# Performance work log

Hardware: AMD Instinct MI355X
Metric: run time of the kernel (lower is better)

## Reference

```python
import jax, jax.numpy as jnp
import numpy as np

KS = 3   # kernel_size
PAD = 1  # padding
N_K = KS * KS


def conv2d(x, w, b=None, stride=1, pad=0):
    out = jax.lax.conv_general_dilated(
        x, w, (stride, stride), [(pad, pad), (pad, pad)],
        dimension_numbers=('NCHW', 'OIHW', 'NCHW'))
    if b is not None:
        out = out + b[None, :, None, None]
    return out


def deform_sample(x, offset):
    # x: [b,c,H,W]  offset: [b,2N,h,w] -> [b,c,h,w,N]
    b, c, H, W = x.shape
    _, twoN, h, w = offset.shape
    N = twoN // 2
    xp = jnp.pad(x, ((0, 0), (0, 0), (PAD, PAD), (PAD, PAD)))
    Hp, Wp = H + 2 * PAD, W + 2 * PAD
    r = (KS - 1) // 2
    knx, kny = jnp.meshgrid(jnp.arange(-r, r + 1), jnp.arange(-r, r + 1), indexing='ij')
    pnx = knx.reshape(-1).astype(offset.dtype)  # [N] kernel x offsets
    pny = kny.reshape(-1).astype(offset.dtype)
    off = jnp.transpose(offset, (0, 2, 3, 1))   # [b,h,w,2N]
    p0x = (jnp.arange(h) + PAD).astype(offset.dtype)
    p0y = (jnp.arange(w) + PAD).astype(offset.dtype)
    px = p0x[None, :, None, None] + pnx[None, None, None, :] + off[..., :N]  # [b,h,w,N]
    py = p0y[None, None, :, None] + pny[None, None, None, :] + off[..., N:]
    # q = p.detach().floor() in torch -> stop_gradient here
    flx = jnp.floor(jax.lax.stop_gradient(px))
    fly = jnp.floor(jax.lax.stop_gradient(py))
    qltx = jnp.clip(flx, 0, Hp - 1)
    qrbx = jnp.clip(flx + 1, 0, Hp - 1)
    qlty = jnp.clip(fly, 0, Wp - 1)
    qrby = jnp.clip(fly + 1, 0, Wp - 1)
    pxc = jnp.clip(px, 0, Hp - 1)
    pyc = jnp.clip(py, 0, Wp - 1)
    g_lt = (1 + (qltx - pxc)) * (1 + (qlty - pyc))
    g_rb = (1 - (qrbx - pxc)) * (1 - (qrby - pyc))
    g_lb = (1 - (qrbx - pxc)) * (1 + (qlty - pyc))
    g_rt = (1 + (qltx - pxc)) * (1 - (qrby - pyc))
    ix_lt, ix_rb = qltx.astype(jnp.int32), qrbx.astype(jnp.int32)
    iy_lt, iy_rb = qlty.astype(jnp.int32), qrby.astype(jnp.int32)

    def gather(ix, iy):
        def one(xb, ixb, iyb):
            return xb[:, ixb, iyb]  # [c,h,w,N]
        return jax.vmap(one)(xp, ix, iy)

    x_lt = gather(ix_lt, iy_lt)
    x_rb = gather(ix_rb, iy_rb)
    x_lb = gather(ix_rb, iy_lt)
    x_rt = gather(ix_lt, iy_rb)
    return (g_lt[:, None] * x_lt + g_rb[:, None] * x_rb
            + g_lb[:, None] * x_lb + g_rt[:, None] * x_rt)


def z_weight(z, mode):
    # cubic interpolation basis weights; z: [b,N,h,w] -> [b,1,h,w,N]
    if mode == '1':
        w = 1 - 11.0 / 6.0 * z + z ** 2 - 1.0 / 6.0 * z ** 3
    elif mode == '2':
        w = 3 * z - 2.5 * z ** 2 + 0.5 * z ** 3
    elif mode == '4':
        w = -1.5 * z + 2 * z ** 2 - 0.5 * z ** 3
    else:
        w = 1.0 / 3.0 * z - 0.5 * z ** 2 + 1.0 / 6.0 * z ** 3
    return jnp.transpose(w, (0, 2, 3, 1))[:, None]


def reshape_x_offset(xo):
    # [b,c,h,w,ks*ks] -> [b,c,h*ks,w*ks] (torch cat/view equivalent)
    b, c, h, w, _ = xo.shape
    xo = xo.reshape(b, c, h, w, KS, KS)          # N = g*ks + k
    xo = jnp.transpose(xo, (0, 1, 2, 4, 3, 5))   # (b,c,h,g,w,k)
    return xo.reshape(b, c, h * KS, w * KS)


def setup_inputs() -> dict:
    key = jax.random.key(0)
    ks = jax.random.split(key, 18)
    B, C, OSC, OUTC, H, W = 2, 64, 64, 64, 128, 128
    f = jax.random.normal
    inp = {
        'img1': f(ks[0], (B, C, H, W), jnp.float32),
        'img2': f(ks[1], (B, C, H, W), jnp.float32),
        'img4': f(ks[2], (B, C, H, W), jnp.float32),
        'img5': f(ks[3], (B, C, H, W), jnp.float32),
        'offset_source': f(ks[4], (B, OSC, H, W), jnp.float32),
        'w_pc1': f(ks[5], (2 * N_K, OSC, 5, 5), jnp.float32) * 0.01,
        'b_pc1': f(ks[6], (2 * N_K,), jnp.float32) * 0.01,
        'w_pc2': f(ks[7], (2 * N_K, OSC, 5, 5), jnp.float32) * 0.01,
        'b_pc2': f(ks[8], (2 * N_K,), jnp.float32) * 0.01,
        'w_pc4': f(ks[9], (2 * N_K, OSC, 5, 5), jnp.float32) * 0.01,
        'b_pc4': f(ks[10], (2 * N_K,), jnp.float32) * 0.01,
        'w_pc5': f(ks[11], (2 * N_K, OSC, 5, 5), jnp.float32) * 0.01,
        'b_pc5': f(ks[12], (2 * N_K,), jnp.float32) * 0.01,
        'w_z': f(ks[13], (N_K, OSC, 5, 5), jnp.float32) * 0.01,
        'b_z': f(ks[14], (N_K,), jnp.float32) * 0.01,
        'w_m': f(ks[15], (N_K, OSC, 5, 5), jnp.float32) * 0.01,
        'b_m': f(ks[16], (N_K,), jnp.float32) * 0.01,
        'w_conv': f(ks[17], (OUTC, C, KS, KS), jnp.float32) * 0.05,
    }
    return inp


def reference(img1, img2, img4, img5, offset_source,
              w_pc1, b_pc1, w_pc2, b_pc2, w_pc4, b_pc4, w_pc5, b_pc5,
              w_z, b_z, w_m, b_m, w_conv):
    off1 = conv2d(offset_source, w_pc1, b_pc1, pad=2)
    off2 = conv2d(offset_source, w_pc2, b_pc2, pad=2)
    off4 = conv2d(offset_source, w_pc4, b_pc4, pad=2)
    off5 = conv2d(offset_source, w_pc5, b_pc5, pad=2)
    z = 3.0 * jax.nn.sigmoid(conv2d(offset_source, w_z, b_z, pad=2))
    m = jax.nn.sigmoid(conv2d(offset_source, w_m, b_m, pad=2))
    f1 = deform_sample(img1, off1)
    f2 = deform_sample(img2, off2)
    f4 = deform_sample(img4, off4)
    f5 = deform_sample(img5, off5)
    central = (f1 * z_weight(z, '1') + f2 * z_weight(z, '2')
               + f4 * z_weight(z, '4') + f5 * z_weight(z, '5'))
    central = central * jnp.transpose(m, (0, 2, 3, 1))[:, None]
    out = conv2d(reshape_x_offset(central), w_conv, None, stride=KS)
    return out
```

## Files before the change

kernel.cpp:

```cpp
#include <hip/hip_runtime.h>
#include <hip/hip_bf16.h>
#include <math.h>

#define HWX 16384

typedef __attribute__((ext_vector_type(8))) short short8v;
typedef __attribute__((ext_vector_type(4))) float f32x4;

__device__ inline ushort f2bf(float x) {
    union { __hip_bfloat16 h; ushort u; } cv;
    cv.h = __float2bfloat16(x);
    return cv.u;
}

__global__ __launch_bounds__(256) void packw_kernel(
    const float* __restrict__ w1, const float* __restrict__ b1,
    const float* __restrict__ w2, const float* __restrict__ b2,
    const float* __restrict__ w4, const float* __restrict__ b4,
    const float* __restrict__ w5, const float* __restrict__ b5,
    const float* __restrict__ wz, const float* __restrict__ bz,
    const float* __restrict__ wm, const float* __restrict__ bm,
    __hip_bfloat16* __restrict__ Wpk, float* __restrict__ bpack)
{
    const int idx = blockIdx.x * 256 + threadIdx.x;
    if (idx < 96) {
        const int o = idx; float v = 0.f;
        if      (o < 18) v = b1[o];
        else if (o < 36) v = b2[o - 18];
        else if (o < 54) v = b4[o - 36];
        else if (o < 72) v = b5[o - 54];
        else if (o < 81) v = bz[o - 72];
        else if (o < 90) v = bm[o - 81];
        bpack[o] = v;
    }
    if (idx < 96 * 1600) {
        const int o   = idx / 1600;
        const int k   = idx - o * 1600;
        const int kyx = k >> 6;
        const int ic  = k & 63;
        const int off = ic * 25 + kyx;
        float v = 0.f;
        if      (o < 18) v = w1[o * 1600 + off];
        else if (o < 36) v = w2[(o - 18) * 1600 + off];
        else if (o < 54) v = w4[(o - 36) * 1600 + off];
        else if (o < 72) v = w5[(o - 54) * 1600 + off];
        else if (o < 81) v = wz[(o - 72) * 1600 + off];
        else if (o < 90) v = wm[(o - 81) * 1600 + off];
        Wpk[idx] = __float2bfloat16(v);
    }
}

__global__ __launch_bounds__(256) void packosT_kernel(
    const float* __restrict__ src, __hip_bfloat16* __restrict__ osT)
{
    const int yy = blockIdx.x;
    const int b  = blockIdx.y;
    __hip_bfloat16* dst = osT + ((size_t)b * 132 + yy) * 132 * 64;
    for (int idx = threadIdx.x; idx < 132 * 64; idx += 256) {
        const int xx = idx >> 6;
        const int c  = idx & 63;
        float v = 0.f;
        if (yy >= 2 && yy < 130 && xx >= 2 && xx < 130)
            v = src[(((b << 6) + c) << 14) + ((yy - 2) << 7) + (xx - 2)];
        dst[idx] = __float2bfloat16(v);
    }
}

__global__ __launch_bounds__(256) void conv_mfma_kernel(
    const __hip_bfloat16* __restrict__ Wpk,
    const float* __restrict__ bpack,
    const __hip_bfloat16* __restrict__ osT,
    float* __restrict__ offs,
    float* __restrict__ zbuf,
    float* __restrict__ mbuf)
{
    __shared__ __align__(16) ushort slab[5 * 68 * 64];
    __shared__ __align__(16) ushort wbuf[2][96 * 64];

    const int bx = blockIdx.x;
    const int y  = bx >> 1;
    const int x0 = (bx & 1) << 6;
    const int b  = blockIdx.y;
    const int t    = threadIdx.x;
    const int wv   = t >> 6;
    const int lane = t & 63;
    const int l15  = lane & 15;
    const int kgrp = lane >> 4;
    const int wm   = wv >> 1;
    const int wn   = wv & 1;

    const ushort* ob = (const ushort*)osT + (size_t)b * (132 * 132 * 64);
    const ushort* Wg = (const ushort*)Wpk;

    for (int c = t; c < 2720; c += 256) {
        const int r5  = c / 544;
        const int rem = c - r5 * 544;
        const int col = rem >> 3;
        const int cb  = rem & 7;
        const short8v v = *(const short8v*)(ob + (((y + r5) * 132 + x0 + col) << 6) + (cb << 3));
        const int slot = r5 * 544 + (col << 3) + (cb ^ (col & 7));
        *(short8v*)((char*)slab + slot * 16) = v;
    }

#define STAGE_W(kyx, bi)                                                       \
    _Pragma("unroll")                                                          \
    for (int it = 0; it < 3; ++it) {                                           \
        const int c  = it * 256 + t;                                           \
        const int oc = c >> 3, cb = c & 7;                                     \
        const ushort* src = Wg + oc * 1600 + (kyx) * 64 + ((cb ^ (oc & 7)) << 3); \
        __builtin_amdgcn_global_load_lds(                                      \
            (const __attribute__((address_space(1))) void*)src,                \
            (__attribute__((address_space(3))) void*)((char*)wbuf[bi] + (it * 256 + wv * 64) * 16), \
            16, 0, 0);                                                         \
    }

    STAGE_W(0, 0)
    __syncthreads();

    f32x4 acc[3][2];
    #pragma unroll
    for (int m = 0; m < 3; ++m)
        #pragma unroll
        for (int n = 0; n < 2; ++n) acc[m][n] = (f32x4){0.f, 0.f, 0.f, 0.f};

    for (int kyx = 0; kyx < 25; ++kyx) {
        const int bi = kyx & 1;
        if (kyx < 24) STAGE_W(kyx + 1, bi ^ 1)
        const int ky = kyx / 5, kx = kyx % 5;
        #pragma unroll
        for (int kc = 0; kc < 2; ++kc) {
            const int kcg = (kc << 2) + kgrp;
            short8v af[3], bf[2];
            #pragma unroll
            for (int m = 0; m < 3; ++m) {
                const int oc = wm * 48 + m * 16 + l15;
                af[m] = *(const short8v*)((char*)wbuf[bi] + ((oc << 3) + (kcg ^ (oc & 7))) * 16);
            }
            #pragma unroll
            for (int n = 0; n < 2; ++n) {
                const int col = wn * 32 + n * 16 + l15 + kx;
                bf[n] = *(const short8v*)((char*)slab + ((ky * 68 + col) * 8 + (kcg ^ (col & 7))) * 16);
            }
            #pragma unroll
            for (int m = 0; m < 3; ++m)
                #pragma unroll
                for (int n = 0; n < 2; ++n)
                    acc[m][n] = __builtin_amdgcn_mfma_f32_16x16x32_bf16(af[m], bf[n], acc[m][n], 0, 0, 0);
        }
        __syncthreads();
    }
#undef STAGE_W

    #pragma unroll
    for (int m = 0; m < 3; ++m) {
        const int ocb = wm * 48 + m * 16 + (kgrp << 2);
        #pragma unroll
        for (int n = 0; n < 2; ++n) {
            const int x = x0 + wn * 32 + n * 16 + l15;
            const int p = (y << 7) + x;
            #pragma unroll
            for (int r = 0; r < 4; ++r) {
                const int o = ocb + r;
                const float v = acc[m][n][r] + bpack[o];
                if (o < 72) {
                    const int i = o / 18, ch = o - i * 18;
                    offs[i * (2 * 18 * HWX) + (((b * 18) + ch) << 14) + p] = v;
                } else if (o < 81) {
                    zbuf[((b * 9 + (o - 72)) << 14) + p] = 3.f / (1.f + expf(-v));
                } else if (o < 90) {
                    mbuf[((b * 9 + (o - 81)) << 14) + p] = 1.f / (1.f + expf(-v));
                }
            }
        }
    }
}

__global__ __launch_bounds__(256) void transpose_kernel(
    const float* __restrict__ i0, const float* __restrict__ i1,
    const float* __restrict__ i2, const float* __restrict__ i3,
    ushort* __restrict__ imgT)
{
    const int img = blockIdx.z;
    const int b   = blockIdx.y;
    const int p0  = blockIdx.x << 6;
    const float* src = (img == 0) ? i0 : (img == 1) ? i1 : (img == 2) ? i2 : i3;

    __shared__ float tile[64][65];
    const int t = threadIdx.x;
    const int pp = t & 63, c0 = t >> 6;
    #pragma unroll
    for (int k = 0; k < 16; ++k) {
        const int c = (k << 2) + c0;
        tile[c][pp] = src[(((b << 6) + c) << 14) + p0 + pp];
    }
    __syncthreads();
    const int c2 = t & 31, pl = t >> 5;
    #pragma unroll
    for (int k = 0; k < 8; ++k) {
        const int pi = (k << 3) + pl;
        const uint packed = (uint)f2bf(tile[2 * c2][pi])
                          | ((uint)f2bf(tile[2 * c2 + 1][pi]) << 16);
        *(uint*)(imgT + ((size_t)(((img << 1) + b) << 14) + p0 + pi) * 64 + 2 * c2)
            = packed;
    }
}

__global__ __launch_bounds__(256) void wcpk_kernel(
    const float* __restrict__ wc, __hip_bfloat16* __restrict__ WcPk)
{
    const int idx = blockIdx.x * 256 + threadIdx.x;
    if (idx < 36864) WcPk[idx] = __float2bfloat16(wc[idx]);
}

__global__ __launch_bounds__(256, 5) void fused_kernel(
    const float* __restrict__ offs,
    const float* __restrict__ zbuf,
    const float* __restrict__ mbuf,
    const ushort* __restrict__ imgT,
    const __hip_bfloat16* __restrict__ WcPk,
    float* __restrict__ out)
{
    __shared__ __hip_bfloat16 s_sb[16 * 584];
    __shared__ ushort4 s_ti[16 * 36];
    __shared__ float4  s_tw4[16 * 36];

    const int t   = threadIdx.x;
    const int pid = blockIdx.x;
    const int b   = pid >> 10;
    const int rem = pid & 1023;
    const int h   = rem >> 3;
    const int w0p = (rem & 7) << 4;

    for (int u = t; u < 576; u += 256) {
        const int px   = u / 36;
        const int unit = u - px * 36;
        const int i    = unit / 9;
        const int n    = unit - i * 9;
        const int wcol = w0p + px;
        const int p    = (h << 7) + wcol;

        const float* ob = offs + i * (2 * 18 * HWX) + ((b * 18) << 14);
        const float ox = ob[(n << 14) + p];
        const float oy = ob[((n + 9) << 14) + p];
        const float z  = zbuf[((b * 9 + n) << 14) + p];
        const float mm = mbuf[((b * 9 + n) << 14) + p];

        const float zc0 = (i == 0) ? 1.f : 0.f;
        const float zc1 = (i == 0) ? (-11.f / 6.f) : (i == 1) ? 3.f
                         : (i == 2) ? -1.5f : (1.f / 3.f);
        const float zc2 = (i == 0) ? 1.f : (i == 1) ? -2.5f
                         : (i == 2) ? 2.f : -0.5f;
        const float zc3 = (i == 0) ? (-1.f / 6.f) : (i == 1) ? 0.5f
                         : (i == 2) ? -0.5f : (1.f / 6.f);
        const float zw   = zc0 + z * (zc1 + z * (zc2 + z * zc3));
        const float coef = zw * mm;

        const float pxf = (float)(h + n / 3) + ox;
        const float pyf = (float)(wcol + n % 3) + oy;
        const float flx = floorf(pxf), fly = floorf(pyf);
        const float qltx = fminf(fmaxf(flx, 0.f), 129.f);
        const float qrbx = fminf(fmaxf(flx + 1.f, 0.f), 129.f);
        const float qlty = fminf(fmaxf(fly, 0.f), 129.f);
        const float qrby = fminf(fmaxf(fly + 1.f, 0.f), 129.f);
        const float pxc = fminf(fmaxf(pxf, 0.f), 129.f);
        const float pyc = fminf(fmaxf(pyf, 0.f), 129.f);
        const float gxl = 1.f + (qltx - pxc);
        const float gxr = 1.f - (qrbx - pxc);
        const float gyl = 1.f + (qlty - pyc);
        const float gyr = 1.f - (qrby - pyc);
        const int ixl = (int)qltx, ixr = (int)qrbx;
        const int iyl = (int)qlty, iyr = (int)qrby;

        ushort4 ti; float4 tw;
        auto mk = [&](int qx, int qy, float g, ushort& ii, float& ww) {
            const bool valid = (qx >= 1) && (qx <= 128) && (qy >= 1) && (qy <= 128);
            ii = (ushort)(valid ? (((qx - 1) << 7) + (qy - 1)) : 0);
            ww = valid ? g * coef : 0.f;
        };
        mk(ixl, iyl, gxl * gyl, ti.x, tw.x);
        mk(ixr, iyr, gxr * gyr, ti.y, tw.y);
        mk(ixr, iyl, gxr * gyl, ti.z, tw.z);
        mk(ixl, iyr, gxl * gyr, ti.w, tw.w);
        s_ti[u]  = ti;
        s_tw4[u] = tw;
    }
    __syncthreads();

    const int lane = t & 63;
    const int wv   = t >> 6;
    const int c4   = lane & 15;
    const int pxs  = lane >> 4;
    const int px   = (wv << 2) + pxs;

    f32x4 s4[9];
    #pragma unroll
    for (int n = 0; n < 9; ++n) s4[n] = (f32x4){0.f, 0.f, 0.f, 0.f};

    const int tb = px * 36;
    #pragma unroll 1
    for (int i = 0; i < 4; ++i) {
        const char* ibl = (const char*)(imgT + (((size_t)((i << 1) + b)) << 20)) + (c4 << 3);
        #pragma unroll
        for (int n = 0; n < 9; ++n) {
            const ushort4 tib = s_ti[tb + i * 9 + n];
            const float4  tw  = s_tw4[tb + i * 9 + n];
            {
                const uint2 v = *(const uint2*)(ibl + ((uint)tib.x << 7));
                s4[n].x = fmaf(tw.x, __uint_as_float(v.x << 16),         s4[n].x);
                s4[n].y = fmaf(tw.x, __uint_as_float(v.x & 0xffff0000u), s4[n].y);
                s4[n].z = fmaf(tw.x, __uint_as_float(v.y << 16),         s4[n].z);
                s4[n].w = fmaf(tw.x, __uint_as_float(v.y & 0xffff0000u), s4[n].w);
            }
            {
                const uint2 v = *(const uint2*)(ibl + ((uint)tib.y << 7));
                s4[n].x = fmaf(tw.y, __uint_as_float(v.x << 16),         s4[n].x);
                s4[n].y = fmaf(tw.y, __uint_as_float(v.x & 0xffff0000u), s4[n].y);
                s4[n].z = fmaf(tw.y, __uint_as_float(v.y << 16),         s4[n].z);
                s4[n].w = fmaf(tw.y, __uint_as_float(v.y & 0xffff0000u), s4[n].w);
            }
            {
                const uint2 v = *(const uint2*)(ibl + ((uint)tib.z << 7));
                s4[n].x = fmaf(tw.z, __uint_as_float(v.x << 16),         s4[n].x);
                s4[n].y = fmaf(tw.z, __uint_as_float(v.x & 0xffff0000u), s4[n].y);
                s4[n].z = fmaf(tw.z, __uint_as_float(v.y << 16),         s4[n].z);
                s4[n].w = fmaf(tw.z, __uint_as_float(v.y & 0xffff0000u), s4[n].w);
            }
            {
                const uint2 v = *(const uint2*)(ibl + ((uint)tib.w << 7));
                s4[n].x = fmaf(tw.w, __uint_as_float(v.x << 16),         s4[n].x);
                s4[n].y = fmaf(tw.w, __uint_as_float(v.x & 0xffff0000u), s4[n].y);
                s4[n].z = fmaf(tw.w, __uint_as_float(v.y << 16),         s4[n].z);
                s4[n].w = fmaf(tw.w, __uint_as_float(v.y & 0xffff0000u), s4[n].w);
            }
        }
    }

    uint bufu[18];
    #pragma unroll
    for (int k = 0; k < 18; ++k) {
        const int u0 = 2 * k, u1 = 2 * k + 1;
        const float v0 = s4[u0 % 9][u0 / 9];
        const float v1 = s4[u1 % 9][u1 / 9];
        bufu[k] = (uint)f2bf(v0) | ((uint)f2bf(v1) << 16);
    }
    {
        uint2* dst = (uint2*)((char*)s_sb + px * 1168 + c4 * 72);
        #pragma unroll
        for (int k = 0; k < 9; ++k)
            dst[k] = ((const uint2*)bufu)[k];
    }
    __syncthreads();

    const int l15  = lane & 15;
    const int kgrp = lane >> 4;
    const ushort* Wb = (const ushort*)WcPk + (wv * 16 + l15) * 576 + kgrp * 8;
    const ushort* sb = (const ushort*)s_sb + l15 * 584 + kgrp * 8;

    f32x4 acc = {0.f, 0.f, 0.f, 0.f};
    #pragma unroll
    for (int ks = 0; ks < 18; ++ks) {
        const short8v a  = *(const short8v*)(Wb + ks * 32);
        const short8v bb = *(const short8v*)(sb + ks * 32);
        acc = __builtin_amdgcn_mfma_f32_16x16x32_bf16(a, bb, acc, 0, 0, 0);
    }

    const int p = (h << 7) + w0p + l15;
    #pragma unroll
    for (int r = 0; r < 4; ++r) {
        const int oc = wv * 16 + (kgrp << 2) + r;
        out[(((b << 6) + oc) << 14) + p] = acc[r];
    }
}

extern "C" void kernel_launch(void* const* d_in, const int* in_sizes, int n_in,
                              void* d_out, int out_size, void* d_ws, size_t ws_size,
                              hipStream_t stream) {
    (void)in_sizes; (void)n_in; (void)out_size; (void)ws_size;
    const float* img1  = (const float*)d_in[0];
    const float* img2  = (const float*)d_in[1];
    const float* img4  = (const float*)d_in[2];
    const float* img5  = (const float*)d_in[3];
    const float* osrc  = (const float*)d_in[4];
    const float* w_pc1 = (const float*)d_in[5];
    const float* b_pc1 = (const float*)d_in[6];
    const float* w_pc2 = (const float*)d_in[7];
    const float* b_pc2 = (const float*)d_in[8];
    const float* w_pc4 = (const float*)d_in[9];
    const float* b_pc4 = (const float*)d_in[10];
    const float* w_pc5 = (const float*)d_in[11];
    const float* b_pc5 = (const float*)d_in[12];
    const float* w_z   = (const float*)d_in[13];
    const float* b_z   = (const float*)d_in[14];
    const float* w_m   = (const float*)d_in[15];
    const float* b_m   = (const float*)d_in[16];
    const float* w_cv  = (const float*)d_in[17];
    float* out = (float*)d_out;

    float* wsf  = (float*)d_ws;
    float* offs = wsf;
    float* zbuf = wsf + 4 * 589824;
    float* mbuf = zbuf + 294912;
    float* WcTr = mbuf + 294912;
    float* imgTr = WcTr + 36864;

    __hip_bfloat16* WcPk  = (__hip_bfloat16*)WcTr;
    ushort*         imgTb = (ushort*)imgTr;

    __hip_bfloat16* Wpk   = (__hip_bfloat16*)imgTr;
    float*          bpack = imgTr + 76800;
    __hip_bfloat16* osT   = (__hip_bfloat16*)(imgTr + 76912);

    packw_kernel<<<dim3((96 * 1600 + 255) / 256), 256, 0, stream>>>(
        w_pc1, b_pc1, w_pc2, b_pc2, w_pc4, b_pc4, w_pc5, b_pc5,
        w_z, b_z, w_m, b_m, Wpk, bpack);
    packosT_kernel<<<dim3(132, 2), 256, 0, stream>>>(osrc, osT);
    conv_mfma_kernel<<<dim3(256, 2), 256, 0, stream>>>(
        Wpk, bpack, osT, offs, zbuf, mbuf);
    transpose_kernel<<<dim3(256, 2, 4), 256, 0, stream>>>(img1, img2, img4, img5, imgTb);
    wcpk_kernel<<<dim3(144), 256, 0, stream>>>(w_cv, WcPk);
    fused_kernel<<<dim3(2048), 256, 0, stream>>>(offs, zbuf, mbuf, imgTb, WcPk, out);
}
```

Before: 118.4 us.

## Swizzle block IDs for XCD locality and pack bilinear taps into bf16

Remaps block indices in the transpose and fused kernels so consecutive work items land on the same XCD (blockIdx & 7 chooses the chunk), so each XCD's L2 holds one batch's image slice and its gathered neighbours. Also packs the four tap indices and four bilinear weights into one uint4 per tap, with the weights stored as bf16, which halves the shared-memory footprint and LDS reads in the gather loop. Rounding the weights to bf16 adds extra precision loss on top of the existing bf16 image data.

```diff
diff --git a/kernel.cpp b/kernel.cpp
--- a/kernel.cpp
+++ b/kernel.cpp
@@ -180,9 +180,12 @@
     const float* __restrict__ i2, const float* __restrict__ i3,
     ushort* __restrict__ imgT)
 {
-    const int img = blockIdx.z;
-    const int b   = blockIdx.y;
-    const int p0  = blockIdx.x << 6;
+    const int wid = ((blockIdx.x & 7) << 8) + (blockIdx.x >> 3);
+    const int xcd = wid >> 8;
+    const int j   = wid & 255;
+    const int img = j >> 6;
+    const int b   = xcd >> 2;
+    const int p0  = ((((xcd & 3) << 6) + (j & 63)) << 6);
     const float* src = (img == 0) ? i0 : (img == 1) ? i1 : (img == 2) ? i2 : i3;
 
     __shared__ float tile[64][65];
@@ -221,11 +224,10 @@
     float* __restrict__ out)
 {
     __shared__ __hip_bfloat16 s_sb[16 * 584];
-    __shared__ ushort4 s_ti[16 * 36];
-    __shared__ float4  s_tw4[16 * 36];
+    __shared__ uint4 s_tap[16 * 36];
 
     const int t   = threadIdx.x;
-    const int pid = blockIdx.x;
+    const int pid = ((blockIdx.x & 7) << 8) + (blockIdx.x >> 3);
     const int b   = pid >> 10;
     const int rem = pid & 1023;
     const int h   = rem >> 3;
@@ -271,18 +273,22 @@
         const int ixl = (int)qltx, ixr = (int)qrbx;
         const int iyl = (int)qlty, iyr = (int)qrby;
 
-        ushort4 ti; float4 tw;
-        auto mk = [&](int qx, int qy, float g, ushort& ii, float& ww) {
+        uint i0, i1, i2, i3, u0, u1, u2, u3;
+        auto mk = [&](int qx, int qy, float g, uint& ii, uint& ww) {
             const bool valid = (qx >= 1) && (qx <= 128) && (qy >= 1) && (qy <= 128);
-            ii = (ushort)(valid ? (((qx - 1) << 7) + (qy - 1)) : 0);
-            ww = valid ? g * coef : 0.f;
+            ii = valid ? (uint)(((qx - 1) << 7) + (qy - 1)) : 0u;
+            ww = valid ? (uint)f2bf(g * coef) : 0u;
         };
-        mk(ixl, iyl, gxl * gyl, ti.x, tw.x);
-        mk(ixr, iyr, gxr * gyr, ti.y, tw.y);
-        mk(ixr, iyl, gxr * gyl, ti.z, tw.z);
-        mk(ixl, iyr, gxl * gyr, ti.w, tw.w);
-        s_ti[u]  = ti;
-        s_tw4[u] = tw;
+        mk(ixl, iyl, gxl * gyl, i0, u0);
+        mk(ixr, iyr, gxr * gyr, i1, u1);
+        mk(ixr, iyl, gxr * gyl, i2, u2);
+        mk(ixl, iyr, gxl * gyr, i3, u3);
+        uint4 tp;
+        tp.x = i0 | (i1 << 16);
+        tp.y = i2 | (i3 << 16);
+        tp.z = u0 | (u1 << 16);
+        tp.w = u2 | (u3 << 16);
+        s_tap[u] = tp;
     }
     __syncthreads();
 
@@ -302,35 +308,38 @@
         const char* ibl = (const char*)(imgT + (((size_t)((i << 1) + b)) << 20)) + (c4 << 3);
         #pragma unroll
         for (int n = 0; n < 9; ++n) {
-            const ushort4 tib = s_ti[tb + i * 9 + n];
-            const float4  tw  = s_tw4[tb + i * 9 + n];
+            const uint4 tp = s_tap[tb + i * 9 + n];
+            const float w0 = __uint_as_float(tp.z << 16);
+            const float w1 = __uint_as_float(tp.z & 0xffff0000u);
+            const float w2 = __uint_as_float(tp.w << 16);
+            const float w3 = __uint_as_float(tp.w & 0xffff0000u);
             {
-                const uint2 v = *(const uint2*)(ibl + ((uint)tib.x << 7));
-                s4[n].x = fmaf(tw.x, __uint_as_float(v.x << 16),         s4[n].x);
-                s4[n].y = fmaf(tw.x, __uint_as_float(v.x & 0xffff0000u), s4[n].y);
-                s4[n].z = fmaf(tw.x, __uint_as_float(v.y << 16),         s4[n].z);
-                s4[n].w = fmaf(tw.x, __uint_as_float(v.y & 0xffff0000u), s4[n].w);
+                const uint2 v = *(const uint2*)(ibl + ((tp.x & 0xffffu) << 7));
+                s4[n].x = fmaf(w0, __uint_as_float(v.x << 16),         s4[n].x);
+                s4[n].y = fmaf(w0, __uint_as_float(v.x & 0xffff0000u), s4[n].y);
+                s4[n].z = fmaf(w0, __uint_as_float(v.y << 16),         s4[n].z);
+                s4[n].w = fmaf(w0, __uint_as_float(v.y & 0xffff0000u), s4[n].w);
             }
             {
-                const uint2 v = *(const uint2*)(ibl + ((uint)tib.y << 7));
-                s4[n].x = fmaf(tw.y, __uint_as_float(v.x << 16),         s4[n].x);
-                s4[n].y = fmaf(tw.y, __uint_as_float(v.x & 0xffff0000u), s4[n].y);
-                s4[n].z = fmaf(tw.y, __uint_as_float(v.y << 16),         s4[n].z);
-                s4[n].w = fmaf(tw.y, __uint_as_float(v.y & 0xffff0000u), s4[n].w);
+                const uint2 v = *(const uint2*)(ibl + ((tp.x >> 16) << 7));
+                s4[n].x = fmaf(w1, __uint_as_float(v.x << 16),         s4[n].x);
+                s4[n].y = fmaf(w1, __uint_as_float(v.x & 0xffff0000u), s4[n].y);
+                s4[n].z = fmaf(w1, __uint_as_float(v.y << 16),         s4[n].z);
+                s4[n].w = fmaf(w1, __uint_as_float(v.y & 0xffff0000u), s4[n].w);
             }
             {
-                const uint2 v = *(const uint2*)(ibl + ((uint)tib.z << 7));
-                s4[n].x = fmaf(tw.z, __uint_as_float(v.x << 16),         s4[n].x);
-                s4[n].y = fmaf(tw.z, __uint_as_float(v.x & 0xffff0000u), s4[n].y);
-                s4[n].z = fmaf(tw.z, __uint_as_float(v.y << 16),         s4[n].z);
-                s4[n].w = fmaf(tw.z, __uint_as_float(v.y & 0xffff0000u), s4[n].w);
+                const uint2 v = *(const uint2*)(ibl + ((tp.y & 0xffffu) << 7));
+                s4[n].x = fmaf(w2, __uint_as_float(v.x << 16),         s4[n].x);
+                s4[n].y = fmaf(w2, __uint_as_float(v.x & 0xffff0000u), s4[n].y);
+                s4[n].z = fmaf(w2, __uint_as_float(v.y << 16),         s4[n].z);
+                s4[n].w = fmaf(w2, __uint_as_float(v.y & 0xffff0000u), s4[n].w);
             }
             {
-                const uint2 v = *(const uint2*)(ibl + ((uint)tib.w << 7));
-                s4[n].x = fmaf(tw.w, __uint_as_float(v.x << 16),         s4[n].x);
-                s4[n].y = fmaf(tw.w, __uint_as_float(v.x & 0xffff0000u), s4[n].y);
-                s4[n].z = fmaf(tw.w, __uint_as_float(v.y << 16),         s4[n].z);
-                s4[n].w = fmaf(tw.w, __uint_as_float(v.y & 0xffff0000u), s4[n].w);
+                const uint2 v = *(const uint2*)(ibl + ((tp.y >> 16) << 7));
+                s4[n].x = fmaf(w3, __uint_as_float(v.x << 16),         s4[n].x);
+                s4[n].y = fmaf(w3, __uint_as_float(v.x & 0xffff0000u), s4[n].y);
+                s4[n].z = fmaf(w3, __uint_as_float(v.y << 16),         s4[n].z);
+                s4[n].w = fmaf(w3, __uint_as_float(v.y & 0xffff0000u), s4[n].w);
             }
         }
     }
@@ -416,7 +425,7 @@
     packosT_kernel<<<dim3(132, 2), 256, 0, stream>>>(osrc, osT);
     conv_mfma_kernel<<<dim3(256, 2), 256, 0, stream>>>(
         Wpk, bpack, osT, offs, zbuf, mbuf);
-    transpose_kernel<<<dim3(256, 2, 4), 256, 0, stream>>>(img1, img2, img4, img5, imgTb);
+    transpose_kernel<<<dim3(2048), 256, 0, stream>>>(img1, img2, img4, img5, imgTb);
     wcpk_kernel<<<dim3(144), 256, 0, stream>>>(w_cv, WcPk);
     fused_kernel<<<dim3(2048), 256, 0, stream>>>(offs, zbuf, mbuf, imgTb, WcPk, out);
 }
```

Measured after the change: 124.3 us. 1.05x slower.

## Split fused gather+GEMM into separate gather and MFMA kernels, pack tap weights as bf16

Applied to the files above, without the earlier changes.

When the workspace is large enough, the fused deformable-sample plus output-conv kernel is split in two. A gather kernel writes the sampled bf16 columns to global memory with an XOR swizzle. An sgemm kernel then loads those columns into LDS via global_load_lds and runs the MFMA reduction. Tap indices and weights are now packed into one uint4 per tap, with the weights in bf16, which halves LDS tap storage but lowers the precision of the bilinear weights. The split adds a roughly 38MB global round trip and an extra launch, in exchange for lower register and LDS pressure in each kernel.

```diff
diff --git a/kernel.cpp b/kernel.cpp
--- a/kernel.cpp
+++ b/kernel.cpp
@@ -70,9 +70,7 @@
     const __hip_bfloat16* __restrict__ Wpk,
     const float* __restrict__ bpack,
     const __hip_bfloat16* __restrict__ osT,
-    float* __restrict__ offs,
-    float* __restrict__ zbuf,
-    float* __restrict__ mbuf)
+    float* __restrict__ offs, float* __restrict__ zbuf, float* __restrict__ mbuf)
 {
     __shared__ __align__(16) ushort slab[5 * 68 * 64];
     __shared__ __align__(16) ushort wbuf[2][96 * 64];
@@ -212,17 +210,121 @@
     if (idx < 36864) WcPk[idx] = __float2bfloat16(wc[idx]);
 }
 
-__global__ __launch_bounds__(256, 5) void fused_kernel(
-    const float* __restrict__ offs,
-    const float* __restrict__ zbuf,
-    const float* __restrict__ mbuf,
-    const ushort* __restrict__ imgT,
-    const __hip_bfloat16* __restrict__ WcPk,
-    float* __restrict__ out)
-{
-    __shared__ __hip_bfloat16 s_sb[16 * 584];
-    __shared__ ushort4 s_ti[16 * 36];
-    __shared__ float4  s_tw4[16 * 36];
+#define TAP_PHASE_A(S_TAP)                                                     \
+    for (int u = t; u < 576; u += 256) {                                       \
+        const int px_  = u / 36;                                               \
+        const int unit = u - px_ * 36;                                         \
+        const int i    = unit / 9;                                             \
+        const int n    = unit - i * 9;                                         \
+        const int wcol = w0p + px_;                                            \
+        const int p    = (h << 7) + wcol;                                      \
+        const float* ob = offs + i * (2 * 18 * HWX) + ((b * 18) << 14);        \
+        const float ox = ob[(n << 14) + p];                                    \
+        const float oy = ob[((n + 9) << 14) + p];                              \
+        const float z  = zbuf[((b * 9 + n) << 14) + p];                        \
+        const float mm = mbuf[((b * 9 + n) << 14) + p];                        \
+        const float zc0 = (i == 0) ? 1.f : 0.f;                                \
+        const float zc1 = (i == 0) ? (-11.f / 6.f) : (i == 1) ? 3.f            \
+                         : (i == 2) ? -1.5f : (1.f / 3.f);                     \
+        const float zc2 = (i == 0) ? 1.f : (i == 1) ? -2.5f                    \
+                         : (i == 2) ? 2.f : -0.5f;                             \
+        const float zc3 = (i == 0) ? (-1.f / 6.f) : (i == 1) ? 0.5f            \
+                         : (i == 2) ? -0.5f : (1.f / 6.f);                     \
+        const float zw   = zc0 + z * (zc1 + z * (zc2 + z * zc3));              \
+        const float coef = zw * mm;                                            \
+        const float pxf = (float)(h + n / 3) + ox;                             \
+        const float pyf = (float)(wcol + n % 3) + oy;                          \
+        const float flx = floorf(pxf), fly = floorf(pyf);                      \
+        const float qltx = fminf(fmaxf(flx, 0.f), 129.f);                      \
+        const float qrbx = fminf(fmaxf(flx + 1.f, 0.f), 129.f);                \
+        const float qlty = fminf(fmaxf(fly, 0.f), 129.f);                      \
+        const float qrby = fminf(fmaxf(fly + 1.f, 0.f), 129.f);                \
+        const float pxc = fminf(fmaxf(pxf, 0.f), 129.f);                       \
+        const float pyc = fminf(fmaxf(pyf, 0.f), 129.f);                       \
+        const float gxl = 1.f + (qltx - pxc);                                  \
+        const float gxr = 1.f - (qrbx - pxc);                                  \
+        const float gyl = 1.f + (qlty - pyc);                                  \
+        const float gyr = 1.f - (qrby - pyc);                                  \
+        const int ixl = (int)qltx, ixr = (int)qrbx;                            \
+        const int iyl = (int)qlty, iyr = (int)qrby;                            \
+        uint i0_, i1_, i2_, i3_, u0_, u1_, u2_, u3_;                           \
+        auto mk = [&](int qx, int qy, float g, uint& ii, uint& ww) {           \
+            const bool valid = (qx >= 1) && (qx <= 128) && (qy >= 1) && (qy <= 128); \
+            ii = valid ? (uint)(((qx - 1) << 7) + (qy - 1)) : 0u;              \
+            ww = valid ? (uint)f2bf(g * coef) : 0u;                            \
+        };                                                                     \
+        mk(ixl, iyl, gxl * gyl, i0_, u0_);                                     \
+        mk(ixr, iyr, gxr * gyr, i1_, u1_);                                     \
+        mk(ixr, iyl, gxr * gyl, i2_, u2_);                                     \
+        mk(ixl, iyr, gxl * gyr, i3_, u3_);                                     \
+        uint4 tp;                                                              \
+        tp.x = i0_ | (i1_ << 16);                                              \
+        tp.y = i2_ | (i3_ << 16);                                              \
+        tp.z = u0_ | (u1_ << 16);                                              \
+        tp.w = u2_ | (u3_ << 16);                                              \
+        S_TAP[u] = tp;                                                         \
+    }
+
+#define TAP_PHASE_B(S_TAP)                                                     \
+    f32x4 s4[9];                                                               \
+    _Pragma("unroll")                                                          \
+    for (int n = 0; n < 9; ++n) s4[n] = (f32x4){0.f, 0.f, 0.f, 0.f};           \
+    const int tb = px * 36;                                                    \
+    _Pragma("unroll 1")                                                        \
+    for (int i = 0; i < 4; ++i) {                                              \
+        const char* ibl = (const char*)(imgT + (((size_t)((i << 1) + b)) << 20)) + (c4 << 3); \
+        _Pragma("unroll")                                                      \
+        for (int n = 0; n < 9; ++n) {                                          \
+            const uint4 tp = S_TAP[tb + i * 9 + n];                            \
+            const float w0 = __uint_as_float(tp.z << 16);                      \
+            const float w1 = __uint_as_float(tp.z & 0xffff0000u);              \
+            const float w2 = __uint_as_float(tp.w << 16);                      \
+            const float w3 = __uint_as_float(tp.w & 0xffff0000u);              \
+            {                                                                  \
+                const uint2 v = *(const uint2*)(ibl + ((tp.x & 0xffffu) << 7));\
+                s4[n].x = fmaf(w0, __uint_as_float(v.x << 16),         s4[n].x); \
+                s4[n].y = fmaf(w0, __uint_as_float(v.x & 0xffff0000u), s4[n].y); \
+                s4[n].z = fmaf(w0, __uint_as_float(v.y << 16),         s4[n].z); \
+                s4[n].w = fmaf(w0, __uint_as_float(v.y & 0xffff0000u), s4[n].w); \
+            }                                                                  \
+            {                                                                  \
+                const uint2 v = *(const uint2*)(ibl + ((tp.x >> 16) << 7));    \
+                s4[n].x = fmaf(w1, __uint_as_float(v.x << 16),         s4[n].x); \
+                s4[n].y = fmaf(w1, __uint_as_float(v.x & 0xffff0000u), s4[n].y); \
+                s4[n].z = fmaf(w1, __uint_as_float(v.y << 16),         s4[n].z); \
+                s4[n].w = fmaf(w1, __uint_as_float(v.y & 0xffff0000u), s4[n].w); \
+            }                                                                  \
+            {                                                                  \
+                const uint2 v = *(const uint2*)(ibl + ((tp.y & 0xffffu) << 7));\
+                s4[n].x = fmaf(w2, __uint_as_float(v.x << 16),         s4[n].x); \
+                s4[n].y = fmaf(w2, __uint_as_float(v.x & 0xffff0000u), s4[n].y); \
+                s4[n].z = fmaf(w2, __uint_as_float(v.y << 16),         s4[n].z); \
+                s4[n].w = fmaf(w2, __uint_as_float(v.y & 0xffff0000u), s4[n].w); \
+            }                                                                  \
+            {                                                                  \
+                const uint2 v = *(const uint2*)(ibl + ((tp.y >> 16) << 7));    \
+                s4[n].x = fmaf(w3, __uint_as_float(v.x << 16),         s4[n].x); \
+                s4[n].y = fmaf(w3, __uint_as_float(v.x & 0xffff0000u), s4[n].y); \
+                s4[n].z = fmaf(w3, __uint_as_float(v.y << 16),         s4[n].z); \
+                s4[n].w = fmaf(w3, __uint_as_float(v.y & 0xffff0000u), s4[n].w); \
+            }                                                                  \
+        }                                                                      \
+    }                                                                          \
+    uint bufu[18];                                                             \
+    _Pragma("unroll")                                                          \
+    for (int k = 0; k < 18; ++k) {                                             \
+        const int u0 = 2 * k, u1 = 2 * k + 1;                                  \
+        const float v0 = s4[u0 % 9][u0 / 9];                                   \
+        const float v1 = s4[u1 % 9][u1 / 9];                                   \
+        bufu[k] = (uint)f2bf(v0) | ((uint)f2bf(v1) << 16);                     \
+    }
+
+__global__ __launch_bounds__(256) void gather_kernel(
+    const float* __restrict__ offs, const float* __restrict__ zbuf,
+    const float* __restrict__ mbuf, const ushort* __restrict__ imgT,
+    ushort* __restrict__ sbuf)
+{
+    __shared__ uint4 s_tap[16 * 36];
 
     const int t   = threadIdx.x;
     const int pid = blockIdx.x;
@@ -231,59 +333,7 @@
     const int h   = rem >> 3;
     const int w0p = (rem & 7) << 4;
 
-    for (int u = t; u < 576; u += 256) {
-        const int px   = u / 36;
-        const int unit = u - px * 36;
-        const int i    = unit / 9;
-        const int n    = unit - i * 9;
-        const int wcol = w0p + px;
-        const int p    = (h << 7) + wcol;
-
-        const float* ob = offs + i * (2 * 18 * HWX) + ((b * 18) << 14);
-        const float ox = ob[(n << 14) + p];
-        const float oy = ob[((n + 9) << 14) + p];
-        const float z  = zbuf[((b * 9 + n) << 14) + p];
-        const float mm = mbuf[((b * 9 + n) << 14) + p];
-
-        const float zc0 = (i == 0) ? 1.f : 0.f;
-        const float zc1 = (i == 0) ? (-11.f / 6.f) : (i == 1) ? 3.f
-                         : (i == 2) ? -1.5f : (1.f / 3.f);
-        const float zc2 = (i == 0) ? 1.f : (i == 1) ? -2.5f
-                         : (i == 2) ? 2.f : -0.5f;
-        const float zc3 = (i == 0) ? (-1.f / 6.f) : (i == 1) ? 0.5f
-                         : (i == 2) ? -0.5f : (1.f / 6.f);
-        const float zw   = zc0 + z * (zc1 + z * (zc2 + z * zc3));
-        const float coef = zw * mm;
-
-        const float pxf = (float)(h + n / 3) + ox;
-        const float pyf = (float)(wcol + n % 3) + oy;
-        const float flx = floorf(pxf), fly = floorf(pyf);
-        const float qltx = fminf(fmaxf(flx, 0.f), 129.f);
-        const float qrbx = fminf(fmaxf(flx + 1.f, 0.f), 129.f);
-        const float qlty = fminf(fmaxf(fly, 0.f), 129.f);
-        const float qrby = fminf(fmaxf(fly + 1.f, 0.f), 129.f);
-        const float pxc = fminf(fmaxf(pxf, 0.f), 129.f);
-        const float pyc = fminf(fmaxf(pyf, 0.f), 129.f);
-        const float gxl = 1.f + (qltx - pxc);
-        const float gxr = 1.f - (qrbx - pxc);
-        const float gyl = 1.f + (qlty - pyc);
-        const float gyr = 1.f - (qrby - pyc);
-        const int ixl = (int)qltx, ixr = (int)qrbx;
-        const int iyl = (int)qlty, iyr = (int)qrby;
-
-        ushort4 ti; float4 tw;
-        auto mk = [&](int qx, int qy, float g, ushort& ii, float& ww) {
-            const bool valid = (qx >= 1) && (qx <= 128) && (qy >= 1) && (qy <= 128);
-            ii = (ushort)(valid ? (((qx - 1) << 7) + (qy - 1)) : 0);
-            ww = valid ? g * coef : 0.f;
-        };
-        mk(ixl, iyl, gxl * gyl, ti.x, tw.x);
-        mk(ixr, iyr, gxr * gyr, ti.y, tw.y);
-        mk(ixr, iyl, gxr * gyl, ti.z, tw.z);
-        mk(ixl, iyr, gxl * gyr, ti.w, tw.w);
-        s_ti[u]  = ti;
-        s_tw4[u] = tw;
-    }
+    TAP_PHASE_A(s_tap)
     __syncthreads();
 
     const int lane = t & 63;
@@ -292,57 +342,95 @@
     const int pxs  = lane >> 4;
     const int px   = (wv << 2) + pxs;
 
-    f32x4 s4[9];
-    #pragma unroll
-    for (int n = 0; n < 9; ++n) s4[n] = (f32x4){0.f, 0.f, 0.f, 0.f};
-
-    const int tb = px * 36;
-    #pragma unroll 1
-    for (int i = 0; i < 4; ++i) {
-        const char* ibl = (const char*)(imgT + (((size_t)((i << 1) + b)) << 20)) + (c4 << 3);
-        #pragma unroll
-        for (int n = 0; n < 9; ++n) {
-            const ushort4 tib = s_ti[tb + i * 9 + n];
-            const float4  tw  = s_tw4[tb + i * 9 + n];
-            {
-                const uint2 v = *(const uint2*)(ibl + ((uint)tib.x << 7));
-                s4[n].x = fmaf(tw.x, __uint_as_float(v.x << 16),         s4[n].x);
-                s4[n].y = fmaf(tw.x, __uint_as_float(v.x & 0xffff0000u), s4[n].y);
-                s4[n].z = fmaf(tw.x, __uint_as_float(v.y << 16),         s4[n].z);
-                s4[n].w = fmaf(tw.x, __uint_as_float(v.y & 0xffff0000u), s4[n].w);
-            }
-            {
-                const uint2 v = *(const uint2*)(ibl + ((uint)tib.y << 7));
-                s4[n].x = fmaf(tw.y, __uint_as_float(v.x << 16),         s4[n].x);
-                s4[n].y = fmaf(tw.y, __uint_as_float(v.x & 0xffff0000u), s4[n].y);
-                s4[n].z = fmaf(tw.y, __uint_as_float(v.y << 16),         s4[n].z);
-                s4[n].w = fmaf(tw.y, __uint_as_float(v.y & 0xffff0000u), s4[n].w);
-            }
-            {
-                const uint2 v = *(const uint2*)(ibl + ((uint)tib.z << 7));
-                s4[n].x = fmaf(tw.z, __uint_as_float(v.x << 16),         s4[n].x);
-                s4[n].y = fmaf(tw.z, __uint_as_float(v.x & 0xffff0000u), s4[n].y);
-                s4[n].z = fmaf(tw.z, __uint_as_float(v.y << 16),         s4[n].z);
-                s4[n].w = fmaf(tw.z, __uint_as_float(v.y & 0xffff0000u), s4[n].w);
-            }
-            {
-                const uint2 v = *(const uint2*)(ibl + ((uint)tib.w << 7));
-                s4[n].x = fmaf(tw.w, __uint_as_float(v.x << 16),         s4[n].x);
-                s4[n].y = fmaf(tw.w, __uint_as_float(v.x & 0xffff0000u), s4[n].y);
-                s4[n].z = fmaf(tw.w, __uint_as_float(v.y << 16),         s4[n].z);
-                s4[n].w = fmaf(tw.w, __uint_as_float(v.y & 0xffff0000u), s4[n].w);
-            }
-        }
-    }
-
-    uint bufu[18];
-    #pragma unroll
-    for (int k = 0; k < 18; ++k) {
-        const int u0 = 2 * k, u1 = 2 * k + 1;
-        const float v0 = s4[u0 % 9][u0 / 9];
-        const float v1 = s4[u1 % 9][u1 / 9];
-        bufu[k] = (uint)f2bf(v0) | ((uint)f2bf(v1) << 16);
-    }
+    TAP_PHASE_B(s_tap)
+
+    char* row = (char*)sbuf + ((size_t)((b << 14) + (h << 7) + w0p + px)) * 1152;
+    const int swz = (px & 7) << 4;
+    #pragma unroll
+    for (int k = 0; k < 9; ++k)
+        *(uint2*)(row + ((c4 * 72 + k * 8) ^ swz)) = ((const uint2*)bufu)[k];
+}
+
+__global__ __launch_bounds__(256) void sgemm_kernel(
+    const ushort* __restrict__ sbuf,
+    const __hip_bfloat16* __restrict__ WcPk,
+    float* __restrict__ out)
+{
+    __shared__ __align__(16) ushort s_sb[16 * 576];
+
+    const int t   = threadIdx.x;
+    const int pid = blockIdx.x;
+    const int b   = pid >> 10;
+    const int rem = pid & 1023;
+    const int h   = rem >> 3;
+    const int w0p = (rem & 7) << 4;
+    const int wv  = t >> 6;
+
+    const char* src = (const char*)sbuf + ((size_t)((b << 14) + (h << 7) + w0p)) * 1152;
+    #pragma unroll
+    for (int k = 0; k < 4; ++k) {
+        __builtin_amdgcn_global_load_lds(
+            (const __attribute__((address_space(1))) void*)(src + (size_t)(k * 256 + t) * 16),
+            (__attribute__((address_space(3))) void*)((char*)s_sb + (k * 256 + wv * 64) * 16),
+            16, 0, 0);
+    }
+    if (t < 128) {
+        __builtin_amdgcn_global_load_lds(
+            (const __attribute__((address_space(1))) void*)(src + (size_t)(1024 + t) * 16),
+            (__attribute__((address_space(3))) void*)((char*)s_sb + (1024 + wv * 64) * 16),
+            16, 0, 0);
+    }
+    __syncthreads();
+
+    const int lane = t & 63;
+    const int l15  = lane & 15;
+    const int kgrp = lane >> 4;
+    const ushort* Wb = (const ushort*)WcPk + (wv * 16 + l15) * 576 + kgrp * 8;
+    const char* sbase = (const char*)s_sb + l15 * 1152;
+    const int swz = (l15 & 7) << 4;
+
+    f32x4 acc = {0.f, 0.f, 0.f, 0.f};
+    #pragma unroll
+    for (int ks = 0; ks < 18; ++ks) {
+        const short8v a  = *(const short8v*)(Wb + ks * 32);
+        const short8v bb = *(const short8v*)(sbase + ((ks * 64 + kgrp * 16) ^ swz));
+        acc = __builtin_amdgcn_mfma_f32_16x16x32_bf16(a, bb, acc, 0, 0, 0);
+    }
+
+    const int p = (h << 7) + w0p + l15;
+    #pragma unroll
+    for (int r = 0; r < 4; ++r) {
+        const int oc = wv * 16 + (kgrp << 2) + r;
+        out[(((b << 6) + oc) << 14) + p] = acc[r];
+    }
+}
+
+__global__ __launch_bounds__(256, 5) void fused_kernel(
+    const float* __restrict__ offs, const float* __restrict__ zbuf,
+    const float* __restrict__ mbuf, const ushort* __restrict__ imgT,
+    const __hip_bfloat16* __restrict__ WcPk, float* __restrict__ out)
+{
+    __shared__ __hip_bfloat16 s_sb[16 * 584];
+    __shared__ uint4 s_tap[16 * 36];
+
+    const int t   = threadIdx.x;
+    const int pid = blockIdx.x;
+    const int b   = pid >> 10;
+    const int rem = pid & 1023;
+    const int h   = rem >> 3;
+    const int w0p = (rem & 7) << 4;
+
+    TAP_PHASE_A(s_tap)
+    __syncthreads();
+
+    const int lane = t & 63;
+    const int wv   = t >> 6;
+    const int c4   = lane & 15;
+    const int pxs  = lane >> 4;
+    const int px   = (wv << 2) + pxs;
+
+    TAP_PHASE_B(s_tap)
+
     {
         uint2* dst = (uint2*)((char*)s_sb + px * 1168 + c4 * 72);
         #pragma unroll
@@ -375,7 +463,7 @@
 extern "C" void kernel_launch(void* const* d_in, const int* in_sizes, int n_in,
                               void* d_out, int out_size, void* d_ws, size_t ws_size,
                               hipStream_t stream) {
-    (void)in_sizes; (void)n_in; (void)out_size; (void)ws_size;
+    (void)in_sizes; (void)n_in; (void)out_size;
     const float* img1  = (const float*)d_in[0];
     const float* img2  = (const float*)d_in[1];
     const float* img4  = (const float*)d_in[2];
@@ -402,6 +490,10 @@
     float* mbuf = zbuf + 294912;
     float* WcTr = mbuf + 294912;
     float* imgTr = WcTr + 36864;
+    ushort* sbuf = (ushort*)(wsf + 11374592);
+
+    const size_t NEED = (size_t)11374592 * 4 + (size_t)18874368 * 2;
+    const bool split = (ws_size >= NEED);
 
     __hip_bfloat16* WcPk  = (__hip_bfloat16*)WcTr;
     ushort*         imgTb = (ushort*)imgTr;
@@ -418,5 +510,10 @@
         Wpk, bpack, osT, offs, zbuf, mbuf);
     transpose_kernel<<<dim3(256, 2, 4), 256, 0, stream>>>(img1, img2, img4, img5, imgTb);
     wcpk_kernel<<<dim3(144), 256, 0, stream>>>(w_cv, WcPk);
-    fused_kernel<<<dim3(2048), 256, 0, stream>>>(offs, zbuf, mbuf, imgTb, WcPk, out);
-}
+    if (split) {
+        gather_kernel<<<dim3(2048), 256, 0, stream>>>(offs, zbuf, mbuf, imgTb, sbuf);
+        sgemm_kernel<<<dim3(2048), 256, 0, stream>>>(sbuf, WcPk, out);
+    } else {
+        fused_kernel<<<dim3(2048), 256, 0, stream>>>(offs, zbuf, mbuf, imgTb, WcPk, out);
+    }
+}
```

After: 140.9 us. +19.0%, slower.

## Pipeline deformable gathers via direct global-to-LDS loads with larger pixel tiles

Applied to the files above, without the earlier changes.

Rewrites the fused sampling+conv kernel so the bilinear tap gathers use global_load_lds DMA into a per-wave LDS ring, software-pipelined three stages deep with explicit vmcnt waits. Each lane now handles 8 channels instead of 4, and each block handles 32 pixels and issues two MFMAs per weight fragment, halving the grid. Tap weights are packed to bf16 alongside their indices, and the conv weight layout is permuted to (n,c) order to match. LDS use grows substantially (64KB raw buffer), which lowers occupancy, and the bf16 tap weights cost some precision.

```diff
diff --git a/kernel.cpp b/kernel.cpp
--- a/kernel.cpp
+++ b/kernel.cpp
@@ -70,9 +70,7 @@
     const __hip_bfloat16* __restrict__ Wpk,
     const float* __restrict__ bpack,
     const __hip_bfloat16* __restrict__ osT,
-    float* __restrict__ offs,
-    float* __restrict__ zbuf,
-    float* __restrict__ mbuf)
+    float* __restrict__ offs, float* __restrict__ zbuf, float* __restrict__ mbuf)
 {
     __shared__ __align__(16) ushort slab[5 * 68 * 64];
     __shared__ __align__(16) ushort wbuf[2][96 * 64];
@@ -209,10 +207,16 @@
     const float* __restrict__ wc, __hip_bfloat16* __restrict__ WcPk)
 {
     const int idx = blockIdx.x * 256 + threadIdx.x;
-    if (idx < 36864) WcPk[idx] = __float2bfloat16(wc[idx]);
-}
-
-__global__ __launch_bounds__(256, 5) void fused_kernel(
+    if (idx < 36864) {
+        const int oc  = idx / 576;
+        const int cnp = idx - oc * 576;
+        const int n   = cnp >> 6;
+        const int c   = cnp & 63;
+        WcPk[idx] = __float2bfloat16(wc[oc * 576 + c * 9 + n]);
+    }
+}
+
+__global__ __launch_bounds__(256) void fused_dma_kernel(
     const float* __restrict__ offs,
     const float* __restrict__ zbuf,
     const float* __restrict__ mbuf,
@@ -220,23 +224,23 @@
     const __hip_bfloat16* __restrict__ WcPk,
     float* __restrict__ out)
 {
-    __shared__ __hip_bfloat16 s_sb[16 * 584];
-    __shared__ ushort4 s_ti[16 * 36];
-    __shared__ float4  s_tw4[16 * 36];
+    __shared__ __align__(16) uint4  s_tap[32 * 36];
+    __shared__ __align__(16) ushort s_sb[32 * 584];
+    __shared__ __align__(16) char   s_raw[4 * 16384];
 
     const int t   = threadIdx.x;
     const int pid = blockIdx.x;
-    const int b   = pid >> 10;
-    const int rem = pid & 1023;
-    const int h   = rem >> 3;
-    const int w0p = (rem & 7) << 4;
-
-    for (int u = t; u < 576; u += 256) {
-        const int px   = u / 36;
-        const int unit = u - px * 36;
+    const int b   = pid >> 9;
+    const int rem = pid & 511;
+    const int h   = rem >> 2;
+    const int w0p = (rem & 3) << 5;
+
+    for (int u = t; u < 1152; u += 256) {
+        const int px_  = u / 36;
+        const int unit = u - px_ * 36;
         const int i    = unit / 9;
         const int n    = unit - i * 9;
-        const int wcol = w0p + px;
+        const int wcol = w0p + px_;
         const int p    = (h << 7) + wcol;
 
         const float* ob = offs + i * (2 * 18 * HWX) + ((b * 18) << 14);
@@ -271,104 +275,128 @@
         const int ixl = (int)qltx, ixr = (int)qrbx;
         const int iyl = (int)qlty, iyr = (int)qrby;
 
-        ushort4 ti; float4 tw;
-        auto mk = [&](int qx, int qy, float g, ushort& ii, float& ww) {
+        uint i0_, i1_, i2_, i3_, u0_, u1_, u2_, u3_;
+        auto mk = [&](int qx, int qy, float g, uint& ii, uint& ww) {
             const bool valid = (qx >= 1) && (qx <= 128) && (qy >= 1) && (qy <= 128);
-            ii = (ushort)(valid ? (((qx - 1) << 7) + (qy - 1)) : 0);
-            ww = valid ? g * coef : 0.f;
+            ii = valid ? (uint)(((qx - 1) << 7) + (qy - 1)) : 0u;
+            ww = valid ? (uint)f2bf(g * coef) : 0u;
         };
-        mk(ixl, iyl, gxl * gyl, ti.x, tw.x);
-        mk(ixr, iyr, gxr * gyr, ti.y, tw.y);
-        mk(ixr, iyl, gxr * gyl, ti.z, tw.z);
-        mk(ixl, iyr, gxl * gyr, ti.w, tw.w);
-        s_ti[u]  = ti;
-        s_tw4[u] = tw;
+        mk(ixl, iyl, gxl * gyl, i0_, u0_);
+        mk(ixr, iyr, gxr * gyr, i1_, u1_);
+        mk(ixr, iyl, gxr * gyl, i2_, u2_);
+        mk(ixl, iyr, gxl * gyr, i3_, u3_);
+        uint4 tp;
+        tp.x = i0_ | (i1_ << 16);
+        tp.y = i2_ | (i3_ << 16);
+        tp.z = u0_ | (u1_ << 16);
+        tp.w = u2_ | (u3_ << 16);
+        s_tap[u] = tp;
     }
     __syncthreads();
 
     const int lane = t & 63;
     const int wv   = t >> 6;
-    const int c4   = lane & 15;
-    const int pxs  = lane >> 4;
-    const int px   = (wv << 2) + pxs;
-
-    f32x4 s4[9];
-    #pragma unroll
-    for (int n = 0; n < 9; ++n) s4[n] = (f32x4){0.f, 0.f, 0.f, 0.f};
-
-    const int tb = px * 36;
-    #pragma unroll 1
-    for (int i = 0; i < 4; ++i) {
-        const char* ibl = (const char*)(imgT + (((size_t)((i << 1) + b)) << 20)) + (c4 << 3);
-        #pragma unroll
-        for (int n = 0; n < 9; ++n) {
-            const ushort4 tib = s_ti[tb + i * 9 + n];
-            const float4  tw  = s_tw4[tb + i * 9 + n];
-            {
-                const uint2 v = *(const uint2*)(ibl + ((uint)tib.x << 7));
-                s4[n].x = fmaf(tw.x, __uint_as_float(v.x << 16),         s4[n].x);
-                s4[n].y = fmaf(tw.x, __uint_as_float(v.x & 0xffff0000u), s4[n].y);
-                s4[n].z = fmaf(tw.x, __uint_as_float(v.y << 16),         s4[n].z);
-                s4[n].w = fmaf(tw.x, __uint_as_float(v.y & 0xffff0000u), s4[n].w);
-            }
-            {
-                const uint2 v = *(const uint2*)(ibl + ((uint)tib.y << 7));
-                s4[n].x = fmaf(tw.y, __uint_as_float(v.x << 16),         s4[n].x);
-                s4[n].y = fmaf(tw.y, __uint_as_float(v.x & 0xffff0000u), s4[n].y);
-                s4[n].z = fmaf(tw.y, __uint_as_float(v.y << 16),         s4[n].z);
-                s4[n].w = fmaf(tw.y, __uint_as_float(v.y & 0xffff0000u), s4[n].w);
-            }
-            {
-                const uint2 v = *(const uint2*)(ibl + ((uint)tib.z << 7));
-                s4[n].x = fmaf(tw.z, __uint_as_float(v.x << 16),         s4[n].x);
-                s4[n].y = fmaf(tw.z, __uint_as_float(v.x & 0xffff0000u), s4[n].y);
-                s4[n].z = fmaf(tw.z, __uint_as_float(v.y << 16),         s4[n].z);
-                s4[n].w = fmaf(tw.z, __uint_as_float(v.y & 0xffff0000u), s4[n].w);
-            }
-            {
-                const uint2 v = *(const uint2*)(ibl + ((uint)tib.w << 7));
-                s4[n].x = fmaf(tw.w, __uint_as_float(v.x << 16),         s4[n].x);
-                s4[n].y = fmaf(tw.w, __uint_as_float(v.x & 0xffff0000u), s4[n].y);
-                s4[n].z = fmaf(tw.w, __uint_as_float(v.y << 16),         s4[n].z);
-                s4[n].w = fmaf(tw.w, __uint_as_float(v.y & 0xffff0000u), s4[n].w);
-            }
-        }
-    }
-
-    uint bufu[18];
-    #pragma unroll
-    for (int k = 0; k < 18; ++k) {
-        const int u0 = 2 * k, u1 = 2 * k + 1;
-        const float v0 = s4[u0 % 9][u0 / 9];
-        const float v1 = s4[u1 % 9][u1 / 9];
-        bufu[k] = (uint)f2bf(v0) | ((uint)f2bf(v1) << 16);
-    }
-    {
-        uint2* dst = (uint2*)((char*)s_sb + px * 1168 + c4 * 72);
-        #pragma unroll
-        for (int k = 0; k < 9; ++k)
-            dst[k] = ((const uint2*)bufu)[k];
-    }
+    const int c8   = lane & 7;
+    const int pxw  = lane >> 3;
+    const int px   = wv * 8 + pxw;
+    const int tapb = px * 36;
+    char* rawbase = s_raw + wv * 16384;
+
+    float s8[8];
+    #pragma unroll
+    for (int m = 0; m < 8; ++m) s8[m] = 0.f;
+
+#define ISSUE(k) {                                                             \
+        const int n_ = (k) >> 2, i_ = (k) & 3;                                 \
+        const uint4 tp = s_tap[tapb + i_ * 9 + n_];                            \
+        const char* ibl = (const char*)imgT + (((size_t)((i_ << 1) + b)) << 21) + c8 * 16; \
+        char* dst = rawbase + ((k) & 3) * 4096;                                \
+        __builtin_amdgcn_global_load_lds(                                      \
+            (const __attribute__((address_space(1))) void*)(ibl + ((tp.x & 0xffffu) << 7)), \
+            (__attribute__((address_space(3))) void*)(dst), 16, 0, 0);         \
+        __builtin_amdgcn_global_load_lds(                                      \
+            (const __attribute__((address_space(1))) void*)(ibl + ((tp.x >> 16) << 7)),     \
+            (__attribute__((address_space(3))) void*)(dst + 1024), 16, 0, 0);  \
+        __builtin_amdgcn_global_load_lds(                                      \
+            (const __attribute__((address_space(1))) void*)(ibl + ((tp.y & 0xffffu) << 7)), \
+            (__attribute__((address_space(3))) void*)(dst + 2048), 16, 0, 0);  \
+        __builtin_amdgcn_global_load_lds(                                      \
+            (const __attribute__((address_space(1))) void*)(ibl + ((tp.y >> 16) << 7)),     \
+            (__attribute__((address_space(3))) void*)(dst + 3072), 16, 0, 0);  \
+    }
+
+#define PROCESS(k) {                                                           \
+        const int n_ = (k) >> 2, i_ = (k) & 3;                                 \
+        const uint4 tp = s_tap[tapb + i_ * 9 + n_];                            \
+        const char* reg = rawbase + ((k) & 3) * 4096 + lane * 16;              \
+        const float wj[4] = { __uint_as_float(tp.z << 16),                     \
+                              __uint_as_float(tp.z & 0xffff0000u),             \
+                              __uint_as_float(tp.w << 16),                     \
+                              __uint_as_float(tp.w & 0xffff0000u) };           \
+        _Pragma("unroll")                                                      \
+        for (int j = 0; j < 4; ++j) {                                          \
+            const uint4 v = *(const uint4*)(reg + j * 1024);                   \
+            s8[0] = fmaf(wj[j], __uint_as_float(v.x << 16),         s8[0]);    \
+            s8[1] = fmaf(wj[j], __uint_as_float(v.x & 0xffff0000u), s8[1]);    \
+            s8[2] = fmaf(wj[j], __uint_as_float(v.y << 16),         s8[2]);    \
+            s8[3] = fmaf(wj[j], __uint_as_float(v.y & 0xffff0000u), s8[3]);    \
+            s8[4] = fmaf(wj[j], __uint_as_float(v.z << 16),         s8[4]);    \
+            s8[5] = fmaf(wj[j], __uint_as_float(v.z & 0xffff0000u), s8[5]);    \
+            s8[6] = fmaf(wj[j], __uint_as_float(v.w << 16),         s8[6]);    \
+            s8[7] = fmaf(wj[j], __uint_as_float(v.w & 0xffff0000u), s8[7]);    \
+        }                                                                      \
+        if (i_ == 3) {                                                         \
+            uint4 pk;                                                          \
+            pk.x = (uint)f2bf(s8[0]) | ((uint)f2bf(s8[1]) << 16);              \
+            pk.y = (uint)f2bf(s8[2]) | ((uint)f2bf(s8[3]) << 16);              \
+            pk.z = (uint)f2bf(s8[4]) | ((uint)f2bf(s8[5]) << 16);              \
+            pk.w = (uint)f2bf(s8[6]) | ((uint)f2bf(s8[7]) << 16);              \
+            *(uint4*)((char*)s_sb + px * 1168 + n_ * 128 + c8 * 16) = pk;      \
+            _Pragma("unroll")                                                  \
+            for (int m = 0; m < 8; ++m) s8[m] = 0.f;                           \
+        }                                                                      \
+    }
+
+    ISSUE(0) ISSUE(1) ISSUE(2)
+    for (int k = 0; k < 33; ++k) {
+        ISSUE(k + 3)
+        asm volatile("s_waitcnt vmcnt(12)" ::: "memory");
+        PROCESS(k)
+    }
+    asm volatile("s_waitcnt vmcnt(8)" ::: "memory");
+    PROCESS(33)
+    asm volatile("s_waitcnt vmcnt(4)" ::: "memory");
+    PROCESS(34)
+    asm volatile("s_waitcnt vmcnt(0)" ::: "memory");
+    PROCESS(35)
+#undef ISSUE
+#undef PROCESS
     __syncthreads();
 
     const int l15  = lane & 15;
     const int kgrp = lane >> 4;
     const ushort* Wb = (const ushort*)WcPk + (wv * 16 + l15) * 576 + kgrp * 8;
-    const ushort* sb = (const ushort*)s_sb + l15 * 584 + kgrp * 8;
-
-    f32x4 acc = {0.f, 0.f, 0.f, 0.f};
+    const char* sb0 = (char*)s_sb + l15 * 1168 + kgrp * 16;
+    const char* sb1 = (char*)s_sb + (16 + l15) * 1168 + kgrp * 16;
+
+    f32x4 acc0 = {0.f, 0.f, 0.f, 0.f};
+    f32x4 acc1 = {0.f, 0.f, 0.f, 0.f};
     #pragma unroll
     for (int ks = 0; ks < 18; ++ks) {
         const short8v a  = *(const short8v*)(Wb + ks * 32);
-        const short8v bb = *(const short8v*)(sb + ks * 32);
-        acc = __builtin_amdgcn_mfma_f32_16x16x32_bf16(a, bb, acc, 0, 0, 0);
-    }
-
-    const int p = (h << 7) + w0p + l15;
+        const short8v b0 = *(const short8v*)(sb0 + ks * 64);
+        const short8v b1 = *(const short8v*)(sb1 + ks * 64);
+        acc0 = __builtin_amdgcn_mfma_f32_16x16x32_bf16(a, b0, acc0, 0, 0, 0);
+        acc1 = __builtin_amdgcn_mfma_f32_16x16x32_bf16(a, b1, acc1, 0, 0, 0);
+    }
+
+    const int pbase = (h << 7) + w0p;
     #pragma unroll
     for (int r = 0; r < 4; ++r) {
         const int oc = wv * 16 + (kgrp << 2) + r;
-        out[(((b << 6) + oc) << 14) + p] = acc[r];
+        float* orow = out + (((b << 6) + oc) << 14) + pbase;
+        orow[l15]      = acc0[r];
+        orow[16 + l15] = acc1[r];
     }
 }
 
@@ -418,5 +446,5 @@
         Wpk, bpack, osT, offs, zbuf, mbuf);
     transpose_kernel<<<dim3(256, 2, 4), 256, 0, stream>>>(img1, img2, img4, img5, imgTb);
     wcpk_kernel<<<dim3(144), 256, 0, stream>>>(w_cv, WcPk);
-    fused_kernel<<<dim3(2048), 256, 0, stream>>>(offs, zbuf, mbuf, imgTb, WcPk, out);
-}
+    fused_dma_kernel<<<dim3(1024), 256, 0, stream>>>(offs, zbuf, mbuf, imgTb, WcPk, out);
+}
```

New measurement: 150.2 us. +26.9%, slower.
